# Performance work log

Hardware: AMD Instinct MI355X
Metric: run time of the kernel (lower is better)

The kernel has to match this reference:

```python
import jax, jax.numpy as jnp
import numpy as np

NQ, M, ND, N, H, DIM = 32, 32, 200, 160, 768, 128
TEMP = 0.1      # log_softmax temperature
TAU = 0.5       # gumbel-softmax temperature
NEG = -10000.0


def _l2norm(x):
    # F.normalize(p=2, dim=-1) with eps clamp
    n = jnp.maximum(jnp.linalg.norm(x, axis=-1, keepdims=True), 1e-12)
    return x / n


def setup_inputs() -> dict:
    key = jax.random.key(0)
    k1, k2, k3, k4, k5, k6 = jax.random.split(key, 6)
    Q = jax.random.normal(k1, (NQ, M, H), dtype=jnp.float32)
    D = jax.random.normal(k2, (ND, N, H), dtype=jnp.float32)
    q_mask = jax.random.randint(k3, (NQ, M), 0, 2).astype(jnp.float32)
    d_mask = jax.random.randint(k4, (ND, N), 0, 2).astype(jnp.float32)
    # pre-sampled Gumbel(0,1) noise for gumbel_softmax (fixed for determinism)
    u = jax.random.uniform(k5, (NQ, ND, M, N), dtype=jnp.float32,
                           minval=1e-6, maxval=1.0 - 1e-6)
    gumbel_noise = -jnp.log(-jnp.log(u))
    # proj_linear: Linear(768, dim, bias=False)
    W_proj = jax.random.normal(k6, (H, DIM), dtype=jnp.float32) / np.sqrt(H)
    return {"Q": Q, "D": D, "q_mask": q_mask, "d_mask": d_mask,
            "gumbel_noise": gumbel_noise, "W_proj": W_proj}


def reference(Q, D, q_mask, d_mask, gumbel_noise, W_proj):
    # project + L2-normalize token embeddings
    Qp = _l2norm(Q @ W_proj)            # [q, m, dim]
    Dp = _l2norm(D @ W_proj)            # [d, n, dim]

    # pairwise token similarities: [q, d, m, n]
    sim = jnp.einsum('qmh,dnh->qdmn', Qp, Dp)

    dm = d_mask[None, :, None, :]       # [1, d, 1, n]
    sim_masked = sim * dm + (1.0 - dm) * NEG

    logits = jax.nn.log_softmax(sim_masked / TEMP, axis=-1)

    # gumbel_softmax(tau=0.5, hard=True) with straight-through
    y_soft = jax.nn.softmax((logits + gumbel_noise) / TAU, axis=-1)
    idx = jnp.argmax(y_soft, axis=-1)
    y_hard = jax.nn.one_hot(idx, N, dtype=y_soft.dtype)
    y = jax.lax.stop_gradient(y_hard - y_soft) + y_soft

    # select doc token per query token, mask query tokens, sum -> [q, d]
    scores = (y * sim_masked).sum(-1)          # [q, d, m]
    scores = scores * q_mask[:, None, :]
    return scores.sum(-1)                      # [q, d]
```

## Files before the change

### kernel.cpp

```cpp
#include <hip/hip_runtime.h>
#include <math.h>

#define NQ_   32
#define M_    32
#define ND_   200
#define N_    160
#define H_    768
#define DIM_  128
#define DROWS_ (ND_ * N_)
#define QROWS_ (NQ_ * M_)
#define TROWS_ (DROWS_ + QROWS_)

__device__ __forceinline__ void gl_lds16(const float* g, float* l) {
    __builtin_amdgcn_global_load_lds(
        (const __attribute__((address_space(1))) unsigned int*)g,
        (__attribute__((address_space(3))) unsigned int*)l, 16, 0, 0);
}

__global__ __launch_bounds__(128) void proj_kernel(
    const float* __restrict__ Dmat, const float* __restrict__ Qmat,
    const float* __restrict__ W, float* __restrict__ DpT,
    float* __restrict__ QpT)
{
    __shared__ float Xt[16][32];
    __shared__ float Ws[16][128];
    const int tid = threadIdx.x;
    const int rb  = blockIdx.x * 32;
    const int cg  = tid & 15;
    const int rg  = tid >> 4;

    float acc[4][8];
#pragma unroll
    for (int i = 0; i < 4; ++i)
#pragma unroll
        for (int j = 0; j < 8; ++j) acc[i][j] = 0.0f;

    for (int kc = 0; kc < H_; kc += 16) {
        {
            int row = tid >> 2, c4 = tid & 3;
            int r = rb + row;
            const float* xr = (r < DROWS_) ? (Dmat + (size_t)r * H_)
                                           : (Qmat + (size_t)(r - DROWS_) * H_);
            float4 v = *reinterpret_cast<const float4*>(xr + kc + c4 * 4);
            Xt[c4*4+0][row] = v.x;
            Xt[c4*4+1][row] = v.y;
            Xt[c4*4+2][row] = v.z;
            Xt[c4*4+3][row] = v.w;
        }
#pragma unroll
        for (int it = 0; it < 4; ++it) {
            int f = tid + it * 128;
            int wr = f >> 5, wc = f & 31;
            *reinterpret_cast<float4*>(&Ws[wr][wc*4]) =
                *reinterpret_cast<const float4*>(&W[(size_t)(kc + wr) * DIM_ + wc * 4]);
        }
        __syncthreads();
#pragma unroll
        for (int k = 0; k < 16; ++k) {
            float a[4], b[8];
            *reinterpret_cast<float4*>(&a[0]) = *reinterpret_cast<const float4*>(&Xt[k][rg*4]);
            *reinterpret_cast<float4*>(&b[0]) = *reinterpret_cast<const float4*>(&Ws[k][cg*8]);
            *reinterpret_cast<float4*>(&b[4]) = *reinterpret_cast<const float4*>(&Ws[k][cg*8+4]);
#pragma unroll
            for (int i = 0; i < 4; ++i)
#pragma unroll
                for (int j = 0; j < 8; ++j)
                    acc[i][j] = fmaf(a[i], b[j], acc[i][j]);
        }
        __syncthreads();
    }

#pragma unroll
    for (int i = 0; i < 4; ++i) {
        int r = rb + rg * 4 + i;
        float ss = 0.0f;
#pragma unroll
        for (int j = 0; j < 8; ++j) ss = __fadd_rn(ss, __fmul_rn(acc[i][j], acc[i][j]));
        ss = __fadd_rn(ss, __shfl_xor(ss, 1));
        ss = __fadd_rn(ss, __shfl_xor(ss, 2));
        ss = __fadd_rn(ss, __shfl_xor(ss, 4));
        ss = __fadd_rn(ss, __shfl_xor(ss, 8));
        float nrm = fmaxf(sqrtf(ss), 1e-12f);
        if (r < DROWS_) {
            int dd = r / 160, n = r - dd * 160;
            float* o = DpT + (size_t)dd * (DIM_ * N_) + n;
#pragma unroll
            for (int j = 0; j < 8; ++j)
                o[(size_t)(cg*8 + j) * N_] = acc[i][j] / nrm;
        } else {
            int rq = r - DROWS_;
            int qq = rq >> 5, m = rq & 31;
            float* o = QpT + (size_t)qq * (DIM_ * M_) + m;
#pragma unroll
            for (int j = 0; j < 8; ++j)
                o[(size_t)(cg*8 + j) * M_] = acc[i][j] / nrm;
        }
    }
}

__global__ __launch_bounds__(64) void score_kernel(
    const float* __restrict__ QpT, const float* __restrict__ DpT,
    const float* __restrict__ qmask, const float* __restrict__ dmask,
    const float* __restrict__ gum, float* __restrict__ out)
{
    __shared__ float Qt[8][32];
    __shared__ float Dt[8][160];
    const int lane = threadIdx.x;
    const int mg   = lane >> 4;
    const int ng   = lane & 15;
    const int q    = blockIdx.x & 31;
    const int d    = blockIdx.x >> 5;

    const float* Qb = QpT + (size_t)q * (DIM_ * M_);
    const float* Db = DpT + (size_t)d * (DIM_ * N_);

    float acc[8][10];
#pragma unroll
    for (int i = 0; i < 8; ++i)
#pragma unroll
        for (int j = 0; j < 10; ++j) acc[i][j] = 0.0f;

    for (int kc = 0; kc < DIM_; kc += 8) {
        gl_lds16(Qb + kc * M_ + lane * 4, &Qt[0][0]);
#pragma unroll
        for (int c = 0; c < 5; ++c)
            gl_lds16(Db + kc * N_ + c * 256 + lane * 4, &Dt[0][0] + c * 256);
        __syncthreads();
#pragma unroll
        for (int k = 0; k < 8; ++k) {
            float a[8], b[10];
            *reinterpret_cast<float4*>(&a[0]) = *reinterpret_cast<const float4*>(&Qt[k][mg*8]);
            *reinterpret_cast<float4*>(&a[4]) = *reinterpret_cast<const float4*>(&Qt[k][mg*8+4]);
            const float* bp = &Dt[k][ng*10];
#pragma unroll
            for (int j2 = 0; j2 < 5; ++j2)
                *reinterpret_cast<float2*>(&b[j2*2]) = *reinterpret_cast<const float2*>(&bp[j2*2]);
#pragma unroll
            for (int i = 0; i < 8; ++i)
#pragma unroll
                for (int j = 0; j < 10; ++j)
                    acc[i][j] = fmaf(a[i], b[j], acc[i][j]);
        }
        __syncthreads();
    }

    float dmv[10];
#pragma unroll
    for (int j = 0; j < 10; ++j)
        dmv[j] = dmask[(size_t)d * N_ + ng*10 + j];

    const float* gq = gum + ((size_t)q * ND_ + d) * ((size_t)M_ * N_);

    float partial = 0.0f;
#pragma unroll
    for (int i = 0; i < 8; ++i) {
        const int m = mg*8 + i;
        float x[10];
        float mx = -3.402823466e38f;
#pragma unroll
        for (int j = 0; j < 10; ++j) {
            float sm = (dmv[j] != 0.0f) ? acc[i][j] : -10000.0f;
            x[j] = sm / 0.1f;
            mx = fmaxf(mx, x[j]);
        }
        mx = fmaxf(mx, __shfl_xor(mx, 1));
        mx = fmaxf(mx, __shfl_xor(mx, 2));
        mx = fmaxf(mx, __shfl_xor(mx, 4));
        mx = fmaxf(mx, __shfl_xor(mx, 8));

        float se = 0.0f;
#pragma unroll
        for (int j = 0; j < 10; ++j) se = __fadd_rn(se, expf(x[j] - mx));
        se = __fadd_rn(se, __shfl_xor(se, 1));
        se = __fadd_rn(se, __shfl_xor(se, 2));
        se = __fadd_rn(se, __shfl_xor(se, 4));
        se = __fadd_rn(se, __shfl_xor(se, 8));
        const float lse = logf(se);

        float g[10];
        const float2* gp = reinterpret_cast<const float2*>(&gq[(size_t)m * N_ + ng*10]);
#pragma unroll
        for (int j2 = 0; j2 < 5; ++j2)
            *reinterpret_cast<float2*>(&g[j2*2]) = gp[j2];

        float z[10];
        float mz = -3.402823466e38f;
#pragma unroll
        for (int j = 0; j < 10; ++j) {
            z[j] = ((x[j] - mx - lse) + g[j]) / 0.5f;
            mz = fmaxf(mz, z[j]);
        }
        mz = fmaxf(mz, __shfl_xor(mz, 1));
        mz = fmaxf(mz, __shfl_xor(mz, 2));
        mz = fmaxf(mz, __shfl_xor(mz, 4));
        mz = fmaxf(mz, __shfl_xor(mz, 8));

        float e2[10];
        float s2 = 0.0f;
#pragma unroll
        for (int j = 0; j < 10; ++j) { e2[j] = expf(z[j] - mz); s2 = __fadd_rn(s2, e2[j]); }
        s2 = __fadd_rn(s2, __shfl_xor(s2, 1));
        s2 = __fadd_rn(s2, __shfl_xor(s2, 2));
        s2 = __fadd_rn(s2, __shfl_xor(s2, 4));
        s2 = __fadd_rn(s2, __shfl_xor(s2, 8));

        float besty = -1.0f; int bestn = 0x7fffffff; float bests = 0.0f;
#pragma unroll
        for (int j = 0; j < 10; ++j) {
            float y = e2[j] / s2;
            if (y > besty) {
                besty = y;
                bestn = ng*10 + j;
                bests = (dmv[j] != 0.0f) ? acc[i][j] : -10000.0f;
            }
        }
#pragma unroll
        for (int dl = 1; dl < 16; dl <<= 1) {
            float oy = __shfl_xor(besty, dl);
            int   on = __shfl_xor(bestn, dl);
            float os = __shfl_xor(bests, dl);
            if (oy > besty || (oy == besty && on < bestn)) {
                besty = oy; bestn = on; bests = os;
            }
        }
        const float qmv = qmask[q * M_ + m];
        if (ng == 0) partial = __fadd_rn(partial, __fmul_rn(bests, qmv));
    }
    partial = __fadd_rn(partial, __shfl_xor(partial, 16));
    partial = __fadd_rn(partial, __shfl_xor(partial, 32));
    if (lane == 0) out[(size_t)q * ND_ + d] = partial;
}

extern "C" void kernel_launch(void* const* d_in, const int* in_sizes, int n_in,
                              void* d_out, int out_size, void* d_ws, size_t ws_size,
                              hipStream_t stream)
{
    const float* Q   = (const float*)d_in[0];
    const float* D   = (const float*)d_in[1];
    const float* qm  = (const float*)d_in[2];
    const float* dm  = (const float*)d_in[3];
    const float* gum = (const float*)d_in[4];
    const float* W   = (const float*)d_in[5];
    float* out = (float*)d_out;

    float* QpT = (float*)d_ws;
    float* DpT = QpT + (size_t)QROWS_ * DIM_;

    proj_kernel<<<dim3(TROWS_ / 32), dim3(128), 0, stream>>>(D, Q, W, DpT, QpT);
    score_kernel<<<dim3(NQ_ * ND_), dim3(64), 0, stream>>>(QpT, DpT, qm, dm, gum, out);
}
```

Before: 499.1 us.

## Double-buffer LDS tiles, widen score blocks to two waves, prefetch gumbel rows

Both kernels now double-buffer their shared-memory K-chunks, so the loads for the next chunk are issued before the current chunk's FMAs and one barrier per iteration goes away. The projection kernel loads W directly into LDS and writes its normalized outputs as float4 stores. The score kernel uses 128 threads per (q,d) pair, each covering 4 query rows, which halves per-thread accumulators. It also prefetches gumbel rows one iteration ahead and combines the two waves through a small LDS reduction. The aim is to hide global-load latency and raise occupancy, at the cost of more LDS per block and an extra barrier at the end.

```diff
diff --git a/kernel.cpp b/kernel.cpp
--- a/kernel.cpp
+++ b/kernel.cpp
@@ -22,12 +22,20 @@
     const float* __restrict__ W, float* __restrict__ DpT,
     float* __restrict__ QpT)
 {
-    __shared__ float Xt[16][32];
-    __shared__ float Ws[16][128];
-    const int tid = threadIdx.x;
-    const int rb  = blockIdx.x * 32;
-    const int cg  = tid & 15;
-    const int rg  = tid >> 4;
+    __shared__ __align__(16) float Xt[2][16][32];
+    __shared__ __align__(16) float Ws[2][16][128];
+    const int tid  = threadIdx.x;
+    const int lane = tid & 63;
+    const int wv   = tid >> 6;
+    const int rb   = blockIdx.x * 32;
+    const int cg   = tid & 15;
+    const int rg   = tid >> 4;
+    const int xrow = tid >> 2;
+    const int xc4  = tid & 3;
+
+    const int rX = rb + xrow;
+    const float* xr = (rX < DROWS_) ? (Dmat + (size_t)rX * H_)
+                                    : (Qmat + (size_t)(rX - DROWS_) * H_);
 
     float acc[4][8];
 #pragma unroll
@@ -35,44 +43,49 @@
 #pragma unroll
         for (int j = 0; j < 8; ++j) acc[i][j] = 0.0f;
 
-    for (int kc = 0; kc < H_; kc += 16) {
-        {
-            int row = tid >> 2, c4 = tid & 3;
-            int r = rb + row;
-            const float* xr = (r < DROWS_) ? (Dmat + (size_t)r * H_)
-                                           : (Qmat + (size_t)(r - DROWS_) * H_);
-            float4 v = *reinterpret_cast<const float4*>(xr + kc + c4 * 4);
-            Xt[c4*4+0][row] = v.x;
-            Xt[c4*4+1][row] = v.y;
-            Xt[c4*4+2][row] = v.z;
-            Xt[c4*4+3][row] = v.w;
-        }
-#pragma unroll
-        for (int it = 0; it < 4; ++it) {
-            int f = tid + it * 128;
-            int wr = f >> 5, wc = f & 31;
-            *reinterpret_cast<float4*>(&Ws[wr][wc*4]) =
-                *reinterpret_cast<const float4*>(&W[(size_t)(kc + wr) * DIM_ + wc * 4]);
-        }
+#pragma unroll
+    for (int t = 0; t < 4; ++t) {
+        const int part = wv * 4 + t;
+        gl_lds16(W + part * 256 + lane * 4, &Ws[0][0][0] + part * 256);
+    }
+    float4 xreg = *reinterpret_cast<const float4*>(xr + xc4 * 4);
+
+    for (int c = 0; c < 48; ++c) {
+        const int cb = c & 1;
+        Xt[cb][xc4*4+0][xrow] = xreg.x;
+        Xt[cb][xc4*4+1][xrow] = xreg.y;
+        Xt[cb][xc4*4+2][xrow] = xreg.z;
+        Xt[cb][xc4*4+3][xrow] = xreg.w;
         __syncthreads();
+        if (c < 47) {
+            const int kc = (c + 1) * 16;
+            const float* wsrc = W + (size_t)kc * DIM_;
+            float* wdst = &Ws[cb ^ 1][0][0];
+#pragma unroll
+            for (int t = 0; t < 4; ++t) {
+                const int part = wv * 4 + t;
+                gl_lds16(wsrc + part * 256 + lane * 4, wdst + part * 256);
+            }
+            xreg = *reinterpret_cast<const float4*>(xr + kc + xc4 * 4);
+        }
+        __builtin_amdgcn_sched_barrier(0);
 #pragma unroll
         for (int k = 0; k < 16; ++k) {
             float a[4], b[8];
-            *reinterpret_cast<float4*>(&a[0]) = *reinterpret_cast<const float4*>(&Xt[k][rg*4]);
-            *reinterpret_cast<float4*>(&b[0]) = *reinterpret_cast<const float4*>(&Ws[k][cg*8]);
-            *reinterpret_cast<float4*>(&b[4]) = *reinterpret_cast<const float4*>(&Ws[k][cg*8+4]);
+            *reinterpret_cast<float4*>(&a[0]) = *reinterpret_cast<const float4*>(&Xt[cb][k][rg*4]);
+            *reinterpret_cast<float4*>(&b[0]) = *reinterpret_cast<const float4*>(&Ws[cb][k][cg*8]);
+            *reinterpret_cast<float4*>(&b[4]) = *reinterpret_cast<const float4*>(&Ws[cb][k][cg*8+4]);
 #pragma unroll
             for (int i = 0; i < 4; ++i)
 #pragma unroll
                 for (int j = 0; j < 8; ++j)
                     acc[i][j] = fmaf(a[i], b[j], acc[i][j]);
         }
-        __syncthreads();
-    }
-
+    }
+
+    float nrm[4];
 #pragma unroll
     for (int i = 0; i < 4; ++i) {
-        int r = rb + rg * 4 + i;
         float ss = 0.0f;
 #pragma unroll
         for (int j = 0; j < 8; ++j) ss = __fadd_rn(ss, __fmul_rn(acc[i][j], acc[i][j]));
@@ -80,81 +93,129 @@
         ss = __fadd_rn(ss, __shfl_xor(ss, 2));
         ss = __fadd_rn(ss, __shfl_xor(ss, 4));
         ss = __fadd_rn(ss, __shfl_xor(ss, 8));
-        float nrm = fmaxf(sqrtf(ss), 1e-12f);
-        if (r < DROWS_) {
-            int dd = r / 160, n = r - dd * 160;
-            float* o = DpT + (size_t)dd * (DIM_ * N_) + n;
-#pragma unroll
-            for (int j = 0; j < 8; ++j)
-                o[(size_t)(cg*8 + j) * N_] = acc[i][j] / nrm;
-        } else {
-            int rq = r - DROWS_;
-            int qq = rq >> 5, m = rq & 31;
-            float* o = QpT + (size_t)qq * (DIM_ * M_) + m;
-#pragma unroll
-            for (int j = 0; j < 8; ++j)
-                o[(size_t)(cg*8 + j) * M_] = acc[i][j] / nrm;
+        nrm[i] = fmaxf(sqrtf(ss), 1e-12f);
+    }
+
+    if (rb < DROWS_) {
+        const int dd = rb / 160, n0 = rb - dd * 160;
+        float* o = DpT + (size_t)dd * (DIM_ * N_) + n0 + rg * 4;
+#pragma unroll
+        for (int j = 0; j < 8; ++j) {
+            float4 v;
+            v.x = acc[0][j] / nrm[0];
+            v.y = acc[1][j] / nrm[1];
+            v.z = acc[2][j] / nrm[2];
+            v.w = acc[3][j] / nrm[3];
+            *reinterpret_cast<float4*>(o + (size_t)(cg*8 + j) * N_) = v;
+        }
+    } else {
+        const int rq = rb - DROWS_;
+        const int qq = rq >> 5;
+        float* o = QpT + (size_t)qq * (DIM_ * M_) + rg * 4;
+#pragma unroll
+        for (int j = 0; j < 8; ++j) {
+            float4 v;
+            v.x = acc[0][j] / nrm[0];
+            v.y = acc[1][j] / nrm[1];
+            v.z = acc[2][j] / nrm[2];
+            v.w = acc[3][j] / nrm[3];
+            *reinterpret_cast<float4*>(o + (size_t)(cg*8 + j) * M_) = v;
         }
     }
 }
 
-__global__ __launch_bounds__(64) void score_kernel(
+__global__ __launch_bounds__(128) void score_kernel(
     const float* __restrict__ QpT, const float* __restrict__ DpT,
     const float* __restrict__ qmask, const float* __restrict__ dmask,
     const float* __restrict__ gum, float* __restrict__ out)
 {
-    __shared__ float Qt[8][32];
-    __shared__ float Dt[8][160];
-    const int lane = threadIdx.x;
-    const int mg   = lane >> 4;
-    const int ng   = lane & 15;
+    __shared__ __align__(16) float Qt[2][8][32];
+    __shared__ __align__(16) float Dt[2][8][160];
+    __shared__ float red[2];
+    const int tid  = threadIdx.x;
+    const int lane = tid & 63;
+    const int wv   = tid >> 6;
+    const int mg   = tid >> 4;
+    const int ng   = tid & 15;
     const int q    = blockIdx.x & 31;
     const int d    = blockIdx.x >> 5;
 
     const float* Qb = QpT + (size_t)q * (DIM_ * M_);
     const float* Db = DpT + (size_t)d * (DIM_ * N_);
 
-    float acc[8][10];
-#pragma unroll
-    for (int i = 0; i < 8; ++i)
+    float acc[4][10];
+#pragma unroll
+    for (int i = 0; i < 4; ++i)
 #pragma unroll
         for (int j = 0; j < 10; ++j) acc[i][j] = 0.0f;
 
-    for (int kc = 0; kc < DIM_; kc += 8) {
-        gl_lds16(Qb + kc * M_ + lane * 4, &Qt[0][0]);
-#pragma unroll
-        for (int c = 0; c < 5; ++c)
-            gl_lds16(Db + kc * N_ + c * 256 + lane * 4, &Dt[0][0] + c * 256);
+    if (wv == 0) {
+        gl_lds16(Qb + lane * 4, &Qt[0][0][0]);
+        gl_lds16(Db + lane * 4, &Dt[0][0][0]);
+        gl_lds16(Db + 256 + lane * 4, &Dt[0][0][0] + 256);
+    } else {
+        gl_lds16(Db + 512  + lane * 4, &Dt[0][0][0] + 512);
+        gl_lds16(Db + 768  + lane * 4, &Dt[0][0][0] + 768);
+        gl_lds16(Db + 1024 + lane * 4, &Dt[0][0][0] + 1024);
+    }
+
+    for (int c = 0; c < 16; ++c) {
+        const int cb = c & 1;
         __syncthreads();
+        if (c < 15) {
+            const float* qsrc = Qb + (size_t)(c + 1) * 8 * M_;
+            const float* dsrc = Db + (size_t)(c + 1) * 8 * N_;
+            float* qdst = &Qt[cb ^ 1][0][0];
+            float* ddst = &Dt[cb ^ 1][0][0];
+            if (wv == 0) {
+                gl_lds16(qsrc + lane * 4, qdst);
+                gl_lds16(dsrc + lane * 4, ddst);
+                gl_lds16(dsrc + 256 + lane * 4, ddst + 256);
+            } else {
+                gl_lds16(dsrc + 512  + lane * 4, ddst + 512);
+                gl_lds16(dsrc + 768  + lane * 4, ddst + 768);
+                gl_lds16(dsrc + 1024 + lane * 4, ddst + 1024);
+            }
+        }
+        __builtin_amdgcn_sched_barrier(0);
 #pragma unroll
         for (int k = 0; k < 8; ++k) {
-            float a[8], b[10];
-            *reinterpret_cast<float4*>(&a[0]) = *reinterpret_cast<const float4*>(&Qt[k][mg*8]);
-            *reinterpret_cast<float4*>(&a[4]) = *reinterpret_cast<const float4*>(&Qt[k][mg*8+4]);
-            const float* bp = &Dt[k][ng*10];
+            float a[4], b[10];
+            *reinterpret_cast<float4*>(&a[0]) = *reinterpret_cast<const float4*>(&Qt[cb][k][mg*4]);
+            const float* bp = &Dt[cb][k][ng*10];
 #pragma unroll
             for (int j2 = 0; j2 < 5; ++j2)
                 *reinterpret_cast<float2*>(&b[j2*2]) = *reinterpret_cast<const float2*>(&bp[j2*2]);
 #pragma unroll
-            for (int i = 0; i < 8; ++i)
+            for (int i = 0; i < 4; ++i)
 #pragma unroll
                 for (int j = 0; j < 10; ++j)
                     acc[i][j] = fmaf(a[i], b[j], acc[i][j]);
         }
-        __syncthreads();
     }
 
     float dmv[10];
-#pragma unroll
-    for (int j = 0; j < 10; ++j)
-        dmv[j] = dmask[(size_t)d * N_ + ng*10 + j];
+    {
+        const float* dmp = dmask + (size_t)d * N_ + ng * 10;
+#pragma unroll
+        for (int j2 = 0; j2 < 5; ++j2)
+            *reinterpret_cast<float2*>(&dmv[j2*2]) = *reinterpret_cast<const float2*>(&dmp[j2*2]);
+    }
 
     const float* gq = gum + ((size_t)q * ND_ + d) * ((size_t)M_ * N_);
 
+    float g[2][10];
+    {
+        const float2* gp = reinterpret_cast<const float2*>(&gq[(size_t)(mg*4) * N_ + ng*10]);
+#pragma unroll
+        for (int j2 = 0; j2 < 5; ++j2)
+            *reinterpret_cast<float2*>(&g[0][j2*2]) = gp[j2];
+    }
+
     float partial = 0.0f;
 #pragma unroll
-    for (int i = 0; i < 8; ++i) {
-        const int m = mg*8 + i;
+    for (int i = 0; i < 4; ++i) {
+        const int m = mg * 4 + i;
         float x[10];
         float mx = -3.402823466e38f;
 #pragma unroll
@@ -162,6 +223,12 @@
             float sm = (dmv[j] != 0.0f) ? acc[i][j] : -10000.0f;
             x[j] = sm / 0.1f;
             mx = fmaxf(mx, x[j]);
+        }
+        if (i < 3) {
+            const float2* gp = reinterpret_cast<const float2*>(&gq[(size_t)(m + 1) * N_ + ng*10]);
+#pragma unroll
+            for (int j2 = 0; j2 < 5; ++j2)
+                *reinterpret_cast<float2*>(&g[(i+1)&1][j2*2]) = gp[j2];
         }
         mx = fmaxf(mx, __shfl_xor(mx, 1));
         mx = fmaxf(mx, __shfl_xor(mx, 2));
@@ -177,17 +244,11 @@
         se = __fadd_rn(se, __shfl_xor(se, 8));
         const float lse = logf(se);
 
-        float g[10];
-        const float2* gp = reinterpret_cast<const float2*>(&gq[(size_t)m * N_ + ng*10]);
-#pragma unroll
-        for (int j2 = 0; j2 < 5; ++j2)
-            *reinterpret_cast<float2*>(&g[j2*2]) = gp[j2];
-
         float z[10];
         float mz = -3.402823466e38f;
 #pragma unroll
         for (int j = 0; j < 10; ++j) {
-            z[j] = ((x[j] - mx - lse) + g[j]) / 0.5f;
+            z[j] = ((x[j] - mx - lse) + g[i&1][j]) / 0.5f;
             mz = fmaxf(mz, z[j]);
         }
         mz = fmaxf(mz, __shfl_xor(mz, 1));
@@ -228,7 +289,9 @@
     }
     partial = __fadd_rn(partial, __shfl_xor(partial, 16));
     partial = __fadd_rn(partial, __shfl_xor(partial, 32));
-    if (lane == 0) out[(size_t)q * ND_ + d] = partial;
+    if (lane == 0) red[wv] = partial;
+    __syncthreads();
+    if (tid == 0) out[(size_t)q * ND_ + d] = __fadd_rn(red[0], red[1]);
 }
 
 extern "C" void kernel_launch(void* const* d_in, const int* in_sizes, int n_in,
@@ -247,5 +310,5 @@
     float* DpT = QpT + (size_t)QROWS_ * DIM_;
 
     proj_kernel<<<dim3(TROWS_ / 32), dim3(128), 0, stream>>>(D, Q, W, DpT, QpT);
-    score_kernel<<<dim3(NQ_ * ND_), dim3(64), 0, stream>>>(QpT, DpT, qm, dm, gum, out);
+    score_kernel<<<dim3(NQ_ * ND_), dim3(128), 0, stream>>>(QpT, DpT, qm, dm, gum, out);
 }
```

Measured after the change: 509.0 us. Within noise of the previous version (+2.0%).

## Halve projection row tile, load W via global_load_lds, vectorize stores

Applied to the files above, without the earlier changes.

The projection kernel now handles 16 rows per block instead of 32, doubling the grid. This raises parallelism but halves reuse of the W tile. Wave 0 loads the X tile while wave 1 streams the W tile straight into LDS with global_load_lds. Output stores become float2 writes of two adjacent rows. Each block now reloads W for half as many rows, so total W traffic doubles.

```diff
diff --git a/kernel.cpp b/kernel.cpp
--- a/kernel.cpp
+++ b/kernel.cpp
@@ -22,47 +22,49 @@
     const float* __restrict__ W, float* __restrict__ DpT,
     float* __restrict__ QpT)
 {
-    __shared__ float Xt[16][32];
-    __shared__ float Ws[16][128];
-    const int tid = threadIdx.x;
-    const int rb  = blockIdx.x * 32;
-    const int cg  = tid & 15;
-    const int rg  = tid >> 4;
-
-    float acc[4][8];
-#pragma unroll
-    for (int i = 0; i < 4; ++i)
+    __shared__ __align__(16) float Xt[16][16];
+    __shared__ __align__(16) float Ws[16][128];
+    const int tid  = threadIdx.x;
+    const int lane = tid & 63;
+    const int wv   = tid >> 6;
+    const int rb   = blockIdx.x * 16;
+    const int cg   = tid & 15;
+    const int rg   = tid >> 4;
+    const int xrow = lane >> 2;
+    const int xc4  = lane & 3;
+
+    const int rX = rb + xrow;
+    const float* xr_ptr = (rX < DROWS_) ? (Dmat + (size_t)rX * H_)
+                                        : (Qmat + (size_t)(rX - DROWS_) * H_);
+
+    float acc[2][8];
+#pragma unroll
+    for (int i = 0; i < 2; ++i)
 #pragma unroll
         for (int j = 0; j < 8; ++j) acc[i][j] = 0.0f;
 
     for (int kc = 0; kc < H_; kc += 16) {
-        {
-            int row = tid >> 2, c4 = tid & 3;
-            int r = rb + row;
-            const float* xr = (r < DROWS_) ? (Dmat + (size_t)r * H_)
-                                           : (Qmat + (size_t)(r - DROWS_) * H_);
-            float4 v = *reinterpret_cast<const float4*>(xr + kc + c4 * 4);
-            Xt[c4*4+0][row] = v.x;
-            Xt[c4*4+1][row] = v.y;
-            Xt[c4*4+2][row] = v.z;
-            Xt[c4*4+3][row] = v.w;
-        }
-#pragma unroll
-        for (int it = 0; it < 4; ++it) {
-            int f = tid + it * 128;
-            int wr = f >> 5, wc = f & 31;
-            *reinterpret_cast<float4*>(&Ws[wr][wc*4]) =
-                *reinterpret_cast<const float4*>(&W[(size_t)(kc + wr) * DIM_ + wc * 4]);
+        if (wv == 0) {
+            float4 v = *reinterpret_cast<const float4*>(xr_ptr + kc + xc4 * 4);
+            Xt[xc4*4+0][xrow] = v.x;
+            Xt[xc4*4+1][xrow] = v.y;
+            Xt[xc4*4+2][xrow] = v.z;
+            Xt[xc4*4+3][xrow] = v.w;
+        } else {
+            const float* wsrc = W + (size_t)kc * DIM_;
+#pragma unroll
+            for (int t = 0; t < 8; ++t)
+                gl_lds16(wsrc + t * 256 + lane * 4, &Ws[0][0] + t * 256);
         }
         __syncthreads();
 #pragma unroll
         for (int k = 0; k < 16; ++k) {
-            float a[4], b[8];
-            *reinterpret_cast<float4*>(&a[0]) = *reinterpret_cast<const float4*>(&Xt[k][rg*4]);
+            float a[2], b[8];
+            *reinterpret_cast<float2*>(&a[0]) = *reinterpret_cast<const float2*>(&Xt[k][rg*2]);
             *reinterpret_cast<float4*>(&b[0]) = *reinterpret_cast<const float4*>(&Ws[k][cg*8]);
             *reinterpret_cast<float4*>(&b[4]) = *reinterpret_cast<const float4*>(&Ws[k][cg*8+4]);
 #pragma unroll
-            for (int i = 0; i < 4; ++i)
+            for (int i = 0; i < 2; ++i)
 #pragma unroll
                 for (int j = 0; j < 8; ++j)
                     acc[i][j] = fmaf(a[i], b[j], acc[i][j]);
@@ -70,9 +72,9 @@
         __syncthreads();
     }
 
-#pragma unroll
-    for (int i = 0; i < 4; ++i) {
-        int r = rb + rg * 4 + i;
+    float nrm[2];
+#pragma unroll
+    for (int i = 0; i < 2; ++i) {
         float ss = 0.0f;
 #pragma unroll
         for (int j = 0; j < 8; ++j) ss = __fadd_rn(ss, __fmul_rn(acc[i][j], acc[i][j]));
@@ -80,20 +82,29 @@
         ss = __fadd_rn(ss, __shfl_xor(ss, 2));
         ss = __fadd_rn(ss, __shfl_xor(ss, 4));
         ss = __fadd_rn(ss, __shfl_xor(ss, 8));
-        float nrm = fmaxf(sqrtf(ss), 1e-12f);
-        if (r < DROWS_) {
-            int dd = r / 160, n = r - dd * 160;
-            float* o = DpT + (size_t)dd * (DIM_ * N_) + n;
-#pragma unroll
-            for (int j = 0; j < 8; ++j)
-                o[(size_t)(cg*8 + j) * N_] = acc[i][j] / nrm;
-        } else {
-            int rq = r - DROWS_;
-            int qq = rq >> 5, m = rq & 31;
-            float* o = QpT + (size_t)qq * (DIM_ * M_) + m;
-#pragma unroll
-            for (int j = 0; j < 8; ++j)
-                o[(size_t)(cg*8 + j) * M_] = acc[i][j] / nrm;
+        nrm[i] = fmaxf(sqrtf(ss), 1e-12f);
+    }
+
+    if (rb < DROWS_) {
+        const int dd = rb / 160, n0 = rb - dd * 160;
+        float* o = DpT + (size_t)dd * (DIM_ * N_) + n0 + rg * 2;
+#pragma unroll
+        for (int j = 0; j < 8; ++j) {
+            float2 v;
+            v.x = acc[0][j] / nrm[0];
+            v.y = acc[1][j] / nrm[1];
+            *reinterpret_cast<float2*>(o + (size_t)(cg*8 + j) * N_) = v;
+        }
+    } else {
+        const int rq = rb - DROWS_;
+        const int qq = rq >> 5, m0 = rq & 31;
+        float* o = QpT + (size_t)qq * (DIM_ * M_) + m0 + rg * 2;
+#pragma unroll
+        for (int j = 0; j < 8; ++j) {
+            float2 v;
+            v.x = acc[0][j] / nrm[0];
+            v.y = acc[1][j] / nrm[1];
+            *reinterpret_cast<float2*>(o + (size_t)(cg*8 + j) * M_) = v;
         }
     }
 }
@@ -246,6 +257,6 @@
     float* QpT = (float*)d_ws;
     float* DpT = QpT + (size_t)QROWS_ * DIM_;
 
-    proj_kernel<<<dim3(TROWS_ / 32), dim3(128), 0, stream>>>(D, Q, W, DpT, QpT);
+    proj_kernel<<<dim3(TROWS_ / 16), dim3(128), 0, stream>>>(D, Q, W, DpT, QpT);
     score_kernel<<<dim3(NQ_ * ND_), dim3(64), 0, stream>>>(QpT, DpT, qm, dm, gum, out);
 }
```

After: 517.3 us. 3.6% more time.
